# Kernel optimization log

Hardware: AMD Instinct MI355X
Metric: run time of the kernel (lower is better)

The kernel has to match this reference:

```python
import jax, jax.numpy as jnp
import numpy as np

GROUP_SIZE = 128
SCALE_MIN = 1e-8
IN_FEATURES = 4096
OUT_FEATURES = 4096
BATCH, SEQ = 4, 2048


def quantize_literati(weight, scales):
    """w -> sign(w) * clamp(scale) per group of GROUP_SIZE along last dim.
    in_features is divisible by GROUP_SIZE, so no padding branch is needed.
    """
    O, C = weight.shape
    wg = weight.reshape(O, C // GROUP_SIZE, GROUP_SIZE)
    # torch.sign with zeros mapped to +1
    signs = jnp.where(wg >= 0, 1.0, -1.0).astype(weight.dtype)
    s = jnp.maximum(scales, SCALE_MIN)  # (O, num_groups)
    w_q = signs * s[..., None]
    return w_q.reshape(O, C)


def setup_inputs() -> dict:
    key = jax.random.key(0)
    kx, kw = jax.random.split(key)
    x = jax.random.normal(kx, (BATCH, SEQ, IN_FEATURES), dtype=jnp.float32)
    # kaiming_uniform_(a=sqrt(5)) -> U(-1/sqrt(fan_in), 1/sqrt(fan_in))
    bound = 1.0 / np.sqrt(IN_FEATURES)
    weight = jax.random.uniform(kw, (OUT_FEATURES, IN_FEATURES), dtype=jnp.float32,
                                minval=-bound, maxval=bound)
    scales = jnp.full((OUT_FEATURES, IN_FEATURES // GROUP_SIZE), 0.1, dtype=jnp.float32)
    return {"x": x, "weight": weight, "scales": scales}


def reference(x, weight, scales):
    w_q = quantize_literati(weight, scales)
    # F.linear: x @ w_q.T
    return jnp.einsum('bsc,oc->bso', x, w_q)
```

## Files before the change

### kernel.cpp

```cpp
#include <hip/hip_runtime.h>
#include <hip/hip_bf16.h>
#include <stdint.h>
#include <stddef.h>


#define M_DIM 8192
#define N_DIM 4096
#define K_DIM 4096
#define BM 128
#define BN 128
#define BK 64

typedef __bf16 bf16x8 __attribute__((ext_vector_type(8)));
typedef float f32x16 __attribute__((ext_vector_type(16)));

__device__ __forceinline__ void async_copy16(const void* g, void* l) {
  __builtin_amdgcn_global_load_lds((__attribute__((address_space(1))) void*)g,
                                   (__attribute__((address_space(3))) void*)l,
                                   16, 0, 0);
}

#define X_THREADS ((size_t)M_DIM * K_DIM / 16)
#define W_THREADS ((size_t)N_DIM * K_DIM / 16)
__global__ __launch_bounds__(256) void prep_kernel(
    const float* __restrict__ x, const float* __restrict__ w,
    const float* __restrict__ scales, __bf16* __restrict__ xb,
    __bf16* __restrict__ wb) {
  const size_t t = (size_t)blockIdx.x * blockDim.x + threadIdx.x;
  if (t < X_THREADS) {
    const float4* src = (const float4*)x + t * 4;
    bf16x8* dst = (bf16x8*)xb + t * 2;
#pragma unroll
    for (int h = 0; h < 2; ++h) {
      const float4 v0 = src[h * 2 + 0];
      const float4 v1 = src[h * 2 + 1];
      bf16x8 o;
      o[0] = (__bf16)v0.x; o[1] = (__bf16)v0.y;
      o[2] = (__bf16)v0.z; o[3] = (__bf16)v0.w;
      o[4] = (__bf16)v1.x; o[5] = (__bf16)v1.y;
      o[6] = (__bf16)v1.z; o[7] = (__bf16)v1.w;
      dst[h] = o;
    }
  } else {
    const size_t u = t - X_THREADS;
    const size_t idx = u * 16;
    const int o_ = (int)(idx >> 12);
    const int grp = (int)(idx & 4095) >> 7;
    const float s = fmaxf(scales[(o_ << 5) + grp], 1e-8f);
    const float4* src = (const float4*)w + u * 4;
    bf16x8* dst = (bf16x8*)wb + u * 2;
#pragma unroll
    for (int h = 0; h < 2; ++h) {
      const float4 v0 = src[h * 2 + 0];
      const float4 v1 = src[h * 2 + 1];
      bf16x8 q;
      q[0] = (__bf16)((v0.x >= 0.f) ? s : -s);
      q[1] = (__bf16)((v0.y >= 0.f) ? s : -s);
      q[2] = (__bf16)((v0.z >= 0.f) ? s : -s);
      q[3] = (__bf16)((v0.w >= 0.f) ? s : -s);
      q[4] = (__bf16)((v1.x >= 0.f) ? s : -s);
      q[5] = (__bf16)((v1.y >= 0.f) ? s : -s);
      q[6] = (__bf16)((v1.z >= 0.f) ? s : -s);
      q[7] = (__bf16)((v1.w >= 0.f) ? s : -s);
      dst[h] = q;
    }
  }
}

template <bool PRECONV>
__global__ __launch_bounds__(256) void literati_gemm(
    const __bf16* __restrict__ Ab, const __bf16* __restrict__ Bb,
    const float* __restrict__ Af, const float* __restrict__ Bf,
    const float* __restrict__ scales, float* __restrict__ C) {
  __shared__ __align__(16) __bf16 As[BM * BK];
  __shared__ __align__(16) __bf16 Bs[BN * BK];

  const int tid = threadIdx.x;
  const int lane = tid & 63;
  const int wave = tid >> 6;
  const int bn0 = blockIdx.x * BN;
  const int bm0 = blockIdx.y * BM;
  const int wm = (wave >> 1) * 64;
  const int wn = (wave & 1) * 64;

  const int l3 = lane >> 3;
  const int l7 = lane & 7;
  const int kc_sw = l7 ^ l3;

  const int m32 = lane & 31;
  const int hl = lane >> 5;
  const int mx7 = m32 & 7;

  f32x16 acc[2][2];
#pragma unroll
  for (int i = 0; i < 2; ++i)
#pragma unroll
    for (int j = 0; j < 2; ++j)
#pragma unroll
      for (int r = 0; r < 16; ++r) acc[i][j][r] = 0.f;

  for (int k0 = 0; k0 < K_DIM; k0 += BK) {
    if constexpr (PRECONV) {
#pragma unroll
      for (int i = 0; i < 4; ++i) {
        const int c = wave * 4 + i;
        const int row = c * 8 + l3;
        async_copy16(Ab + (size_t)(bm0 + row) * K_DIM + k0 + kc_sw * 8,
                     &As[(c * 64 + lane) * 8]);
      }
#pragma unroll
      for (int i = 0; i < 4; ++i) {
        const int c = wave * 4 + i;
        const int row = c * 8 + l3;
        async_copy16(Bb + (size_t)(bn0 + row) * K_DIM + k0 + kc_sw * 8,
                     &Bs[(c * 64 + lane) * 8]);
      }
      asm volatile("s_waitcnt vmcnt(0)" ::: "memory");
    } else {
#pragma unroll
      for (int i = 0; i < 4; ++i) {
        const int c = wave * 4 + i;
        const int row = c * 8 + l3;
        const float* src = Af + (size_t)(bm0 + row) * K_DIM + k0 + kc_sw * 8;
        const float4 v0 = ((const float4*)src)[0];
        const float4 v1 = ((const float4*)src)[1];
        bf16x8 o;
        o[0] = (__bf16)v0.x; o[1] = (__bf16)v0.y;
        o[2] = (__bf16)v0.z; o[3] = (__bf16)v0.w;
        o[4] = (__bf16)v1.x; o[5] = (__bf16)v1.y;
        o[6] = (__bf16)v1.z; o[7] = (__bf16)v1.w;
        *(bf16x8*)&As[(c * 64 + lane) * 8] = o;
      }
#pragma unroll
      for (int i = 0; i < 4; ++i) {
        const int c = wave * 4 + i;
        const int row = c * 8 + l3;
        const int gr = bn0 + row;
        const float* src = Bf + (size_t)gr * K_DIM + k0 + kc_sw * 8;
        const float s = fmaxf(scales[(gr << 5) + ((k0 + kc_sw * 8) >> 7)], 1e-8f);
        const float4 v0 = ((const float4*)src)[0];
        const float4 v1 = ((const float4*)src)[1];
        bf16x8 o;
        o[0] = (__bf16)((v0.x >= 0.f) ? s : -s);
        o[1] = (__bf16)((v0.y >= 0.f) ? s : -s);
        o[2] = (__bf16)((v0.z >= 0.f) ? s : -s);
        o[3] = (__bf16)((v0.w >= 0.f) ? s : -s);
        o[4] = (__bf16)((v1.x >= 0.f) ? s : -s);
        o[5] = (__bf16)((v1.y >= 0.f) ? s : -s);
        o[6] = (__bf16)((v1.z >= 0.f) ? s : -s);
        o[7] = (__bf16)((v1.w >= 0.f) ? s : -s);
        *(bf16x8*)&Bs[(c * 64 + lane) * 8] = o;
      }
    }
    __syncthreads();

#pragma unroll
    for (int ks = 0; ks < 4; ++ks) {
      bf16x8 av[2], bv[2];
      const int kc = ks * 2 + hl;
#pragma unroll
      for (int i = 0; i < 2; ++i) {
        const int slot = (wm + i * 32 + m32) * 8 + (kc ^ mx7);
        av[i] = *(const bf16x8*)&As[slot * 8];
      }
#pragma unroll
      for (int j = 0; j < 2; ++j) {
        const int slot = (wn + j * 32 + m32) * 8 + (kc ^ mx7);
        bv[j] = *(const bf16x8*)&Bs[slot * 8];
      }
#pragma unroll
      for (int i = 0; i < 2; ++i)
#pragma unroll
        for (int j = 0; j < 2; ++j)
          acc[i][j] = __builtin_amdgcn_mfma_f32_32x32x16_bf16(av[i], bv[j],
                                                              acc[i][j], 0, 0, 0);
    }
    __syncthreads();
  }

#pragma unroll
  for (int i = 0; i < 2; ++i) {
#pragma unroll
    for (int j = 0; j < 2; ++j) {
      const int col = bn0 + wn + j * 32 + m32;
      const int rbase = bm0 + wm + i * 32 + 4 * hl;
#pragma unroll
      for (int r = 0; r < 16; ++r) {
        const int row = rbase + (r & 3) + 8 * (r >> 2);
        C[(size_t)row * N_DIM + col] = acc[i][j][r];
      }
    }
  }
}

extern "C" void kernel_launch(void* const* d_in, const int* in_sizes, int n_in,
                              void* d_out, int out_size, void* d_ws, size_t ws_size,
                              hipStream_t stream) {
  const float* x = (const float*)d_in[0];
  const float* w = (const float*)d_in[1];
  const float* sc = (const float*)d_in[2];
  float* out = (float*)d_out;

  const size_t need = ((size_t)M_DIM + (size_t)N_DIM) * K_DIM * sizeof(__bf16);
  dim3 grid(N_DIM / BN, M_DIM / BM);

  if (ws_size >= need) {
    __bf16* xb = (__bf16*)d_ws;
    __bf16* wb = xb + (size_t)M_DIM * K_DIM;
    const size_t total_threads = X_THREADS + W_THREADS;
    prep_kernel<<<(int)(total_threads / 256), 256, 0, stream>>>(x, w, sc, xb, wb);
    literati_gemm<true><<<grid, 256, 0, stream>>>(xb, wb, nullptr, nullptr,
                                                  nullptr, out);
  } else {
    literati_gemm<false><<<grid, 256, 0, stream>>>(nullptr, nullptr, x, w, sc,
                                                   out);
  }
}
```

Before: 515.7 us.

## Rewrite GEMM with 256x256 tiles, 4-stage async LDS pipeline and 16x16 MFMA

Replaces the single-buffered 128x128 GEMM with a 256x256 block tile on 512 threads. Global-to-LDS async copies run three tiles ahead through four LDS buffers, with split A/B staging interleaved with MFMA phases, s_setprio around compute, and a new XOR swizzle. Uses 16x16x32 bf16 MFMA. The fallback path for a small workspace is removed, so the workspace size is now assumed. 128 KB of LDS per block and heavy register use may limit occupancy below the requested two blocks per CU.

```diff
diff --git a/kernel.cpp b/kernel.cpp
--- a/kernel.cpp
+++ b/kernel.cpp
@@ -7,12 +7,13 @@
 #define M_DIM 8192
 #define N_DIM 4096
 #define K_DIM 4096
-#define BM 128
-#define BN 128
-#define BK 64
+#define BM 256
+#define BN 256
+#define BK 32
+#define NT (K_DIM / BK)
 
 typedef __bf16 bf16x8 __attribute__((ext_vector_type(8)));
-typedef float f32x16 __attribute__((ext_vector_type(16)));
+typedef float f32x4 __attribute__((ext_vector_type(4)));
 
 __device__ __forceinline__ void async_copy16(const void* g, void* l) {
   __builtin_amdgcn_global_load_lds((__attribute__((address_space(1))) void*)g,
@@ -67,152 +68,155 @@
   }
 }
 
-template <bool PRECONV>
-__global__ __launch_bounds__(256) void literati_gemm(
+
+#define LDS_A(b) ((char*)lds + (b) * 32768)
+#define LDS_B(b) ((char*)lds + (b) * 32768 + 16384)
+
+#define STAGE_A(tt) do {                                              \
+    char* _d = LDS_A((tt) & 3);                                       \
+    async_copy16(aS[0] + (size_t)(tt) * BK, _d + dOff[0]);            \
+    async_copy16(aS[1] + (size_t)(tt) * BK, _d + dOff[1]);            \
+  } while (0)
+
+#define STAGE_B(tt) do {                                              \
+    char* _d = LDS_B((tt) & 3);                                       \
+    async_copy16(bS[0] + (size_t)(tt) * BK, _d + dOff[0]);            \
+    async_copy16(bS[1] + (size_t)(tt) * BK, _d + dOff[1]);            \
+  } while (0)
+
+#define TILE_BODY(tt, DO_STAGE, VMSTR) do {                                    \
+    char* _bufA = LDS_A((tt) & 3);                                             \
+    char* _bufB = LDS_B((tt) & 3);                                             \
+    bf16x8 _av[4]; bf16x8 _bv[4];                                              \
+                                             \
+    _Pragma("unroll") for (int _i = 0; _i < 4; ++_i)                           \
+      _av[_i] = *(const bf16x8*)(_bufA + aOff[0][_i]);                         \
+    _Pragma("unroll") for (int _j = 0; _j < 4; ++_j)                           \
+      _bv[_j] = *(const bf16x8*)(_bufB + bOff[_j]);                            \
+    if (DO_STAGE) STAGE_A((tt) + 3);                                           \
+    __builtin_amdgcn_s_barrier();                                              \
+    asm volatile("s_waitcnt lgkmcnt(0)" ::: "memory");                         \
+    __builtin_amdgcn_sched_barrier(0);                                         \
+    __builtin_amdgcn_s_setprio(1);                                             \
+    _Pragma("unroll") for (int _i = 0; _i < 4; ++_i)                           \
+      _Pragma("unroll") for (int _j = 0; _j < 4; ++_j)                         \
+        acc[_i][_j] = __builtin_amdgcn_mfma_f32_16x16x32_bf16(                 \
+            _av[_i], _bv[_j], acc[_i][_j], 0, 0, 0);                           \
+    __builtin_amdgcn_s_setprio(0);                                             \
+    __builtin_amdgcn_s_barrier();                                              \
+                             \
+    _Pragma("unroll") for (int _i = 0; _i < 4; ++_i)                           \
+      _av[_i] = *(const bf16x8*)(_bufA + aOff[1][_i]);                         \
+    if (DO_STAGE) STAGE_B((tt) + 3);                                           \
+    __builtin_amdgcn_s_barrier();                                              \
+    asm volatile("s_waitcnt lgkmcnt(0)" ::: "memory");                         \
+    __builtin_amdgcn_sched_barrier(0);                                         \
+    __builtin_amdgcn_s_setprio(1);                                             \
+    _Pragma("unroll") for (int _i = 0; _i < 4; ++_i)                           \
+      _Pragma("unroll") for (int _j = 0; _j < 4; ++_j)                         \
+        acc[4 + _i][_j] = __builtin_amdgcn_mfma_f32_16x16x32_bf16(             \
+            _av[_i], _bv[_j], acc[4 + _i][_j], 0, 0, 0);                       \
+    __builtin_amdgcn_s_setprio(0);                                             \
+    asm volatile("s_waitcnt " VMSTR ::: "memory");                             \
+    __builtin_amdgcn_s_barrier();                                              \
+  } while (0)
+
+__global__ __launch_bounds__(512, 2) void literati_gemm(
     const __bf16* __restrict__ Ab, const __bf16* __restrict__ Bb,
-    const float* __restrict__ Af, const float* __restrict__ Bf,
-    const float* __restrict__ scales, float* __restrict__ C) {
-  __shared__ __align__(16) __bf16 As[BM * BK];
-  __shared__ __align__(16) __bf16 Bs[BN * BK];
+    float* __restrict__ C) {
+  __shared__ __align__(16) char lds[4 * 32768];
 
   const int tid = threadIdx.x;
   const int lane = tid & 63;
   const int wave = tid >> 6;
   const int bn0 = blockIdx.x * BN;
   const int bm0 = blockIdx.y * BM;
-  const int wm = (wave >> 1) * 64;
-  const int wn = (wave & 1) * 64;
-
-  const int l3 = lane >> 3;
-  const int l7 = lane & 7;
-  const int kc_sw = l7 ^ l3;
-
-  const int m32 = lane & 31;
-  const int hl = lane >> 5;
-  const int mx7 = m32 & 7;
-
-  f32x16 acc[2][2];
-#pragma unroll
-  for (int i = 0; i < 2; ++i)
-#pragma unroll
-    for (int j = 0; j < 2; ++j)
-#pragma unroll
-      for (int r = 0; r < 16; ++r) acc[i][j][r] = 0.f;
-
-  for (int k0 = 0; k0 < K_DIM; k0 += BK) {
-    if constexpr (PRECONV) {
-#pragma unroll
-      for (int i = 0; i < 4; ++i) {
-        const int c = wave * 4 + i;
-        const int row = c * 8 + l3;
-        async_copy16(Ab + (size_t)(bm0 + row) * K_DIM + k0 + kc_sw * 8,
-                     &As[(c * 64 + lane) * 8]);
+  const int wm = wave >> 2;
+  const int wn = wave & 3;
+
+  const int r_in = lane >> 2;
+  const int kc_st = (lane & 3) ^ ((lane >> 3) & 3);
+  const __bf16* aS[2];
+  const __bf16* bS[2];
+  int dOff[2];
+#pragma unroll
+  for (int i = 0; i < 2; ++i) {
+    const int c64 = wave * 2 + i;
+    aS[i] = Ab + (size_t)(bm0 + c64 * 16 + r_in) * K_DIM + kc_st * 8;
+    bS[i] = Bb + (size_t)(bn0 + c64 * 16 + r_in) * K_DIM + kc_st * 8;
+    dOff[i] = (c64 * 64 + lane) * 16;
+  }
+
+  const int fr = lane & 15;
+  const int kc_rd = lane >> 4;
+  int aOff[2][4], bOff[4];
+#pragma unroll
+  for (int mh = 0; mh < 2; ++mh)
+#pragma unroll
+    for (int i = 0; i < 4; ++i) {
+      const int row = wm * 128 + mh * 64 + i * 16 + fr;
+      aOff[mh][i] = (row * 4 + (kc_rd ^ ((row >> 1) & 3))) * 16;
+    }
+#pragma unroll
+  for (int j = 0; j < 4; ++j) {
+    const int row = wn * 64 + j * 16 + fr;
+    bOff[j] = (row * 4 + (kc_rd ^ ((row >> 1) & 3))) * 16;
+  }
+
+  f32x4 acc[8][4];
+#pragma unroll
+  for (int f = 0; f < 8; ++f)
+#pragma unroll
+    for (int j = 0; j < 4; ++j)
+#pragma unroll
+      for (int r = 0; r < 4; ++r) acc[f][j][r] = 0.f;
+
+#pragma unroll
+  for (int tt = 0; tt < 3; ++tt) {
+    STAGE_A(tt);
+    STAGE_B(tt);
+  }
+  asm volatile("s_waitcnt vmcnt(8)" ::: "memory");
+  __builtin_amdgcn_s_barrier();
+
+  for (int t = 0; t < NT - 3; ++t) TILE_BODY(t, 1, "vmcnt(8)");
+  TILE_BODY(NT - 3, 0, "vmcnt(4)");
+  TILE_BODY(NT - 2, 0, "vmcnt(0)");
+  TILE_BODY(NT - 1, 0, "vmcnt(0)");
+
+  const int col0 = bn0 + wn * 64 + fr;
+  const int rbase = bm0 + wm * 128 + (lane >> 4) * 4;
+#pragma unroll
+  for (int mh = 0; mh < 2; ++mh)
+#pragma unroll
+    for (int i = 0; i < 4; ++i) {
+      const int row0 = rbase + mh * 64 + i * 16;
+#pragma unroll
+      for (int j = 0; j < 4; ++j) {
+        float* p = C + (size_t)row0 * N_DIM + col0 + j * 16;
+#pragma unroll
+        for (int r = 0; r < 4; ++r)
+          p[(size_t)r * N_DIM] = acc[mh * 4 + i][j][r];
       }
-#pragma unroll
-      for (int i = 0; i < 4; ++i) {
-        const int c = wave * 4 + i;
-        const int row = c * 8 + l3;
-        async_copy16(Bb + (size_t)(bn0 + row) * K_DIM + k0 + kc_sw * 8,
-                     &Bs[(c * 64 + lane) * 8]);
-      }
-      asm volatile("s_waitcnt vmcnt(0)" ::: "memory");
-    } else {
-#pragma unroll
-      for (int i = 0; i < 4; ++i) {
-        const int c = wave * 4 + i;
-        const int row = c * 8 + l3;
-        const float* src = Af + (size_t)(bm0 + row) * K_DIM + k0 + kc_sw * 8;
-        const float4 v0 = ((const float4*)src)[0];
-        const float4 v1 = ((const float4*)src)[1];
-        bf16x8 o;
-        o[0] = (__bf16)v0.x; o[1] = (__bf16)v0.y;
-        o[2] = (__bf16)v0.z; o[3] = (__bf16)v0.w;
-        o[4] = (__bf16)v1.x; o[5] = (__bf16)v1.y;
-        o[6] = (__bf16)v1.z; o[7] = (__bf16)v1.w;
-        *(bf16x8*)&As[(c * 64 + lane) * 8] = o;
-      }
-#pragma unroll
-      for (int i = 0; i < 4; ++i) {
-        const int c = wave * 4 + i;
-        const int row = c * 8 + l3;
-        const int gr = bn0 + row;
-        const float* src = Bf + (size_t)gr * K_DIM + k0 + kc_sw * 8;
-        const float s = fmaxf(scales[(gr << 5) + ((k0 + kc_sw * 8) >> 7)], 1e-8f);
-        const float4 v0 = ((const float4*)src)[0];
-        const float4 v1 = ((const float4*)src)[1];
-        bf16x8 o;
-        o[0] = (__bf16)((v0.x >= 0.f) ? s : -s);
-        o[1] = (__bf16)((v0.y >= 0.f) ? s : -s);
-        o[2] = (__bf16)((v0.z >= 0.f) ? s : -s);
-        o[3] = (__bf16)((v0.w >= 0.f) ? s : -s);
-        o[4] = (__bf16)((v1.x >= 0.f) ? s : -s);
-        o[5] = (__bf16)((v1.y >= 0.f) ? s : -s);
-        o[6] = (__bf16)((v1.z >= 0.f) ? s : -s);
-        o[7] = (__bf16)((v1.w >= 0.f) ? s : -s);
-        *(bf16x8*)&Bs[(c * 64 + lane) * 8] = o;
-      }
-    }
-    __syncthreads();
-
-#pragma unroll
-    for (int ks = 0; ks < 4; ++ks) {
-      bf16x8 av[2], bv[2];
-      const int kc = ks * 2 + hl;
-#pragma unroll
-      for (int i = 0; i < 2; ++i) {
-        const int slot = (wm + i * 32 + m32) * 8 + (kc ^ mx7);
-        av[i] = *(const bf16x8*)&As[slot * 8];
-      }
-#pragma unroll
-      for (int j = 0; j < 2; ++j) {
-        const int slot = (wn + j * 32 + m32) * 8 + (kc ^ mx7);
-        bv[j] = *(const bf16x8*)&Bs[slot * 8];
-      }
-#pragma unroll
-      for (int i = 0; i < 2; ++i)
-#pragma unroll
-        for (int j = 0; j < 2; ++j)
-          acc[i][j] = __builtin_amdgcn_mfma_f32_32x32x16_bf16(av[i], bv[j],
-                                                              acc[i][j], 0, 0, 0);
-    }
-    __syncthreads();
-  }
-
-#pragma unroll
-  for (int i = 0; i < 2; ++i) {
-#pragma unroll
-    for (int j = 0; j < 2; ++j) {
-      const int col = bn0 + wn + j * 32 + m32;
-      const int rbase = bm0 + wm + i * 32 + 4 * hl;
-#pragma unroll
-      for (int r = 0; r < 16; ++r) {
-        const int row = rbase + (r & 3) + 8 * (r >> 2);
-        C[(size_t)row * N_DIM + col] = acc[i][j][r];
-      }
-    }
-  }
+    }
 }
 
 extern "C" void kernel_launch(void* const* d_in, const int* in_sizes, int n_in,
                               void* d_out, int out_size, void* d_ws, size_t ws_size,
                               hipStream_t stream) {
+  (void)in_sizes; (void)n_in; (void)out_size;
   const float* x = (const float*)d_in[0];
   const float* w = (const float*)d_in[1];
   const float* sc = (const float*)d_in[2];
   float* out = (float*)d_out;
 
-  const size_t need = ((size_t)M_DIM + (size_t)N_DIM) * K_DIM * sizeof(__bf16);
+  __bf16* xb = (__bf16*)d_ws;
+  __bf16* wb = xb + (size_t)M_DIM * K_DIM;
+  (void)ws_size;
+
+  const size_t total_threads = X_THREADS + W_THREADS;
+  prep_kernel<<<(int)(total_threads / 256), 256, 0, stream>>>(x, w, sc, xb, wb);
+
   dim3 grid(N_DIM / BN, M_DIM / BM);
-
-  if (ws_size >= need) {
-    __bf16* xb = (__bf16*)d_ws;
-    __bf16* wb = xb + (size_t)M_DIM * K_DIM;
-    const size_t total_threads = X_THREADS + W_THREADS;
-    prep_kernel<<<(int)(total_threads / 256), 256, 0, stream>>>(x, w, sc, xb, wb);
-    literati_gemm<true><<<grid, 256, 0, stream>>>(xb, wb, nullptr, nullptr,
-                                                  nullptr, out);
-  } else {
-    literati_gemm<false><<<grid, 256, 0, stream>>>(nullptr, nullptr, x, w, sc,
-                                                   out);
-  }
-}
+  literati_gemm<<<grid, 512, 0, stream>>>(xb, wb, out);
+}
```

After: 493.7 us. -4.3%, faster.
